# Kernel tuning notes

Hardware: AMD Instinct MI355X
Metric: run time of the kernel (lower is better)

## Reference

```python
import jax, jax.numpy as jnp
import numpy as np

N_EMBD = 1024
N_HEADS = 16
HEAD_DIM = N_EMBD // N_HEADS


def setup_inputs() -> dict:
    key = jax.random.key(0)
    ks = jax.random.split(key, 5)
    s = 0.02
    return {
        "x": jax.random.normal(ks[0], (4, 2048, N_EMBD), dtype=jnp.float32),
        "w_attn": jax.random.normal(ks[1], (N_EMBD, 3 * N_EMBD), dtype=jnp.float32) * s,
        "b_attn": jnp.zeros((3 * N_EMBD,), dtype=jnp.float32),
        "w_proj": jax.random.normal(ks[2], (N_EMBD, N_EMBD), dtype=jnp.float32) * s,
        "b_proj": jnp.zeros((N_EMBD,), dtype=jnp.float32),
    }


def reference(x, w_attn, b_attn, w_proj, b_proj):
    B, T, C = x.shape
    H, D = N_HEADS, HEAD_DIM
    qkv = x @ w_attn + b_attn                      # [B,T,3C]
    q, k, v = jnp.split(qkv, 3, axis=-1)
    q = q.reshape(B, T, H, D).transpose(0, 2, 1, 3)  # [B,H,T,D]
    k = k.reshape(B, T, H, D).transpose(0, 2, 1, 3)
    v = v.reshape(B, T, H, D).transpose(0, 2, 1, 3)
    # Faithful to source bug: divide by d**(-0.5) == multiply by sqrt(d)
    scale = jnp.asarray(D, x.dtype) ** 0.5
    scores = jnp.einsum("bhqd,bhkd->bhqk", q, k) * scale  # [B,H,T,T]
    causal = jnp.tril(jnp.ones((T, T), dtype=bool))
    scores = jnp.where(causal[None, None], scores, -jnp.inf)
    attn = jax.nn.softmax(scores, axis=-1)
    y = jnp.einsum("bhqk,bhkd->bhqd", attn, v)     # [B,H,T,D]
    y = y.transpose(0, 2, 1, 3).reshape(B, T, C)
    return y @ w_proj + b_proj
```

## Files before the change

### kernel.cpp

```cpp
#include <hip/hip_runtime.h>
#include <cmath>

#define BB 4
#define TT 2048
#define CC 1024
#define HH 16
#define DD 64
#define MM (BB*TT)

typedef _Float16 f16x8 __attribute__((ext_vector_type(8)));
typedef _Float16 f16x4 __attribute__((ext_vector_type(4)));
typedef _Float16 f16x2 __attribute__((ext_vector_type(2)));
typedef float f32x4 __attribute__((ext_vector_type(4)));
typedef unsigned short ushort_t;

#define MFMA16(a,b,c) __builtin_amdgcn_mfma_f32_16x16x16f16(a,b,c,0,0,0)

__device__ __forceinline__ unsigned short f2h(float f) {
    _Float16 h = (_Float16)f;
    return __builtin_bit_cast(unsigned short, h);
}

__device__ __forceinline__ f16x2 cvt_pk(float a, float b) {
    return __builtin_bit_cast(f16x2, __builtin_amdgcn_cvt_pkrtz(a, b));
}

__device__ __forceinline__ void gld16(const void* gsrc, void* ldst) {
    void* g = const_cast<void*>(gsrc);
    __builtin_amdgcn_global_load_lds(
        (__attribute__((address_space(1))) void*)g,
        (__attribute__((address_space(3))) void*)ldst,
        16, 0, 0);
}

__global__ __launch_bounds__(256)
void cvt4_kernel(const float* __restrict__ in, ushort_t* __restrict__ out, long n4) {
    long i = (long)blockIdx.x * blockDim.x + threadIdx.x;
    if (i >= n4) return;
    float4 v = ((const float4*)in)[i];
    ushort4 o;
    o.x = f2h(v.x); o.y = f2h(v.y); o.z = f2h(v.z); o.w = f2h(v.w);
    ((ushort4*)out)[i] = o;
}

__global__ __launch_bounds__(256)
void trcvt_kernel(const float* __restrict__ in, ushort_t* __restrict__ out,
                  int K, int N) {
    __shared__ float T[32][33];
    const int tx = threadIdx.x & 31;
    const int ty = threadIdx.x >> 5;
    const int n0 = blockIdx.x * 32;
    const int k0 = blockIdx.y * 32;
    #pragma unroll
    for (int i = 0; i < 4; ++i)
        T[ty + i * 8][tx] = in[(size_t)(k0 + ty + i * 8) * N + n0 + tx];
    __syncthreads();
    #pragma unroll
    for (int i = 0; i < 4; ++i)
        out[(size_t)(n0 + ty + i * 8) * K + k0 + tx] = f2h(T[tx][ty + i * 8]);
}

template<int N, bool QKV>
__global__ __launch_bounds__(256)
void hgemm_kernel(const ushort_t* __restrict__ A, const ushort_t* __restrict__ Bt,
                  const float* __restrict__ bias, float* __restrict__ out,
                  ushort_t* __restrict__ qh, ushort_t* __restrict__ kh,
                  ushort_t* __restrict__ vh)
{
    const int K = 1024;
    __shared__ ushort_t As[2][128 * 32];
    __shared__ ushort_t Bs[2][128 * 32];

    const int tid  = threadIdx.x;
    const int lane = tid & 63;
    const int wave = tid >> 6;
    const int wm   = (wave & 1) * 64;
    const int wn   = (wave >> 1) * 64;
    const int m0   = blockIdx.y * 128;
    const int n0   = blockIdx.x * 128;
    const int lrow = lane & 15;
    const int quad = lane >> 4;

    unsigned offA[4], offB[4];
    ushort_t* ldsA[4];
    ushort_t* ldsB[4];
    #pragma unroll
    for (int p = 0; p < 4; ++p) {
        const int d   = p * 256 + tid;
        const int blk = d >> 9;
        const int row = (d >> 2) & 127;
        const int c16 = d & 3;
        offA[p] = (unsigned)(m0 + row) * K + blk * 32 + c16 * 8;
        offB[p] = (unsigned)(n0 + row) * K + blk * 32 + c16 * 8;
        ldsA[p] = &As[0][0] + (p * 256 + wave * 64) * 8;
        ldsB[p] = &Bs[0][0] + (p * 256 + wave * 64) * 8;
    }

    f32x4 acc[4][4];
    const f32x4 z = {0.f, 0.f, 0.f, 0.f};
    #pragma unroll
    for (int mt = 0; mt < 4; ++mt)
        #pragma unroll
        for (int nt = 0; nt < 4; ++nt)
            acc[mt][nt] = z;

    for (int kk = 0; kk < K; kk += 64) {
        #pragma unroll
        for (int p = 0; p < 4; ++p) {
            gld16(&A[offA[p] + kk],  ldsA[p]);
            gld16(&Bt[offB[p] + kk], ldsB[p]);
        }
        __syncthreads();

        #pragma unroll
        for (int ks = 0; ks < 2; ++ks) {
            f16x8 af[4], bf[4];
            #pragma unroll
            for (int mt = 0; mt < 4; ++mt)
                af[mt] = *(const f16x8*)&As[ks][(wm + mt * 16 + lrow) * 32 + quad * 8];
            #pragma unroll
            for (int nt = 0; nt < 4; ++nt)
                bf[nt] = *(const f16x8*)&Bs[ks][(wn + nt * 16 + lrow) * 32 + quad * 8];
            #pragma unroll
            for (int mt = 0; mt < 4; ++mt)
                #pragma unroll
                for (int nt = 0; nt < 4; ++nt)
                    acc[mt][nt] = __builtin_amdgcn_mfma_f32_16x16x32_f16(
                        af[mt], bf[nt], acc[mt][nt], 0, 0, 0);
        }
        __syncthreads();
    }

    #pragma unroll
    for (int mt = 0; mt < 4; ++mt) {
        const int rbase = m0 + wm + mt * 16 + quad * 4;
        #pragma unroll
        for (int nt = 0; nt < 4; ++nt) {
            const int col = n0 + wn + nt * 16 + lrow;
            const float bv = bias[col];
            if (QKV) {
                const int which = col >> 10;
                const int c = col & 1023;
                const int h = c >> 6, d = c & 63;
                const int b = rbase >> 11, t0 = rbase & 2047;
                if (which == 2) {
                    ushort4 pk;
                    pk.x = f2h(acc[mt][nt][0] + bv);
                    pk.y = f2h(acc[mt][nt][1] + bv);
                    pk.z = f2h(acc[mt][nt][2] + bv);
                    pk.w = f2h(acc[mt][nt][3] + bv);
                    *(ushort4*)&vh[(((size_t)b * HH + h) * DD + d) * TT + t0] = pk;
                } else {
                    ushort_t* dst = which ? kh : qh;
                    const float sc = which ? 1.0f : 8.0f * 1.44269504088896f;
                    #pragma unroll
                    for (int r = 0; r < 4; ++r)
                        dst[(((size_t)b * HH + h) * TT + t0 + r) * DD + d] =
                            f2h((acc[mt][nt][r] + bv) * sc);
                }
            } else {
                #pragma unroll
                for (int r = 0; r < 4; ++r)
                    out[(size_t)(rbase + r) * N + col] = acc[mt][nt][r] + bv;
            }
        }
    }
}

__global__ __launch_bounds__(256, 4)
void attn_mfma_kernel(const ushort_t* __restrict__ qh, const ushort_t* __restrict__ kh,
                      const ushort_t* __restrict__ vh, ushort_t* __restrict__ yh)
{
    __shared__ ushort_t Ks[2][64 * 72];
    __shared__ ushort_t Vs[2][64 * 72];

    const int pr   = blockIdx.x;
    const int bh   = blockIdx.y;
    const int qtA  = 31 - pr;
    const int qtB  = pr;
    const int tid  = threadIdx.x;
    const int lane = tid & 63;
    const int w    = tid >> 6;
    const int lrow = lane & 15;
    const int quad = lane >> 4;

    const ushort_t* qbase = qh + (size_t)bh * TT * DD;
    const ushort_t* kbase = kh + (size_t)bh * TT * DD;
    const ushort_t* vbase = vh + (size_t)bh * DD * TT;
    const int b = bh >> 4, h = bh & 15;

    const int ur = tid >> 3;
    const int uc = (tid & 7) * 8;

    int q0w = qtA * 64 + w * 16;
    f16x8 aq0 = *(const f16x8*)&qbase[(size_t)(q0w + lrow) * DD + quad * 8];
    f16x8 aq1 = *(const f16x8*)&qbase[(size_t)(q0w + lrow) * DD + 32 + quad * 8];

    const f32x4 z = {0.f, 0.f, 0.f, 0.f};
    f32x4 o[4] = {z, z, z, z};
    float mi = -1e30f, li = 0.f;

    uint4 kr0 = *(const uint4*)&kbase[(size_t)ur * DD + uc];
    uint4 kr1 = *(const uint4*)&kbase[(size_t)(ur + 32) * DD + uc];
    uint4 vr0 = *(const uint4*)&vbase[(size_t)ur * TT + uc];
    uint4 vr1 = *(const uint4*)&vbase[(size_t)(ur + 32) * TT + uc];

    *(uint4*)&Ks[0][(ur)      * 72 + uc] = kr0;
    *(uint4*)&Ks[0][(ur + 32) * 72 + uc] = kr1;
    *(uint4*)&Vs[0][(ur)      * 72 + uc] = vr0;
    *(uint4*)&Vs[0][(ur + 32) * 72 + uc] = vr1;
    {
        const int nkt = (1 <= qtA) ? 1 : 0;
        const int nb  = nkt * 64;
        kr0 = *(const uint4*)&kbase[(size_t)(nb + ur) * DD + uc];
        kr1 = *(const uint4*)&kbase[(size_t)(nb + ur + 32) * DD + uc];
        vr0 = *(const uint4*)&vbase[(size_t)ur * TT + nb + uc];
        vr1 = *(const uint4*)&vbase[(size_t)(ur + 32) * TT + nb + uc];
    }
    __syncthreads();

    for (int i = 0; i <= 32; ++i) {
        const int cur = i & 1;
        if (i == qtA + 1) {
            #pragma unroll
            for (int r = 0; r < 4; ++r) {
                const float inv = 1.0f / __shfl(li, quad * 4 + r, 64);
                const int t = q0w + quad * 4 + r;
                #pragma unroll
                for (int dt = 0; dt < 4; ++dt)
                    yh[((size_t)b * TT + t) * CC + h * 64 + dt * 16 + lrow] =
                        f2h(o[dt][r] * inv);
            }
            q0w = qtB * 64 + w * 16;
            aq0 = *(const f16x8*)&qbase[(size_t)(q0w + lrow) * DD + quad * 8];
            aq1 = *(const f16x8*)&qbase[(size_t)(q0w + lrow) * DD + 32 + quad * 8];
            #pragma unroll
            for (int dt = 0; dt < 4; ++dt) o[dt] = z;
            mi = -1e30f; li = 0.f;
        }
        const int kt = (i <= qtA) ? i : i - qtA - 1;

        f32x4 sv[4];
        __builtin_amdgcn_s_setprio(1);
        #pragma unroll
        for (int c = 0; c < 4; ++c) {
            f16x8 ka = *(const f16x8*)&Ks[cur][(c * 16 + lrow) * 72 + quad * 8];
            f16x8 kb = *(const f16x8*)&Ks[cur][(c * 16 + lrow) * 72 + 32 + quad * 8];
            sv[c] = __builtin_amdgcn_mfma_f32_16x16x32_f16(ka, aq0, z, 0, 0, 0);
            sv[c] = __builtin_amdgcn_mfma_f32_16x16x32_f16(kb, aq1, sv[c], 0, 0, 0);
        }
        __builtin_amdgcn_s_setprio(0);

        const int kt2 = kt * 64;
        const int qg  = q0w + lrow;
        const bool diag = (i == qtA) || (i == 32);
        if (diag) {
            #pragma unroll
            for (int c = 0; c < 4; ++c)
                #pragma unroll
                for (int r = 0; r < 4; ++r)
                    if (kt2 + c * 16 + quad * 4 + r > qg) sv[c][r] = -3e38f;
        }
        float mc[4];
        #pragma unroll
        for (int c = 0; c < 4; ++c)
            mc[c] = fmaxf(fmaxf(sv[c][0], sv[c][1]), fmaxf(sv[c][2], sv[c][3]));
        float m = fmaxf(fmaxf(mc[0], mc[1]), fmaxf(mc[2], mc[3]));
        m = fmaxf(m, __shfl_xor(m, 16, 64));
        m = fmaxf(m, __shfl_xor(m, 32, 64));

        if (__any(m > mi + 8.0f)) {
            const float mnew  = fmaxf(mi, m);
            const float alpha = exp2f(mi - mnew);
            mi = mnew;
            li *= alpha;
            #pragma unroll
            for (int r = 0; r < 4; ++r) {
                const float ar = __shfl(alpha, quad * 4 + r, 64);
                #pragma unroll
                for (int dt = 0; dt < 4; ++dt) o[dt][r] *= ar;
            }
        }

        f16x4 ap[4];
        float rc[4];
        #pragma unroll
        for (int c = 0; c < 4; ++c) {
            const float p0 = exp2f(sv[c][0] - mi);
            const float p1 = exp2f(sv[c][1] - mi);
            const float p2 = exp2f(sv[c][2] - mi);
            const float p3 = exp2f(sv[c][3] - mi);
            rc[c] = (p0 + p1) + (p2 + p3);
            const f16x2 lo = cvt_pk(p0, p1);
            const f16x2 hi = cvt_pk(p2, p3);
            ap[c][0] = lo[0]; ap[c][1] = lo[1]; ap[c][2] = hi[0]; ap[c][3] = hi[1];
        }
        float rs = (rc[0] + rc[1]) + (rc[2] + rc[3]);
        rs += __shfl_xor(rs, 16, 64);
        rs += __shfl_xor(rs, 32, 64);
        li += rs;

        __builtin_amdgcn_s_setprio(1);
        #pragma unroll
        for (int dt = 0; dt < 4; ++dt)
            #pragma unroll
            for (int c = 0; c < 4; ++c) {
                f16x4 vb = *(const f16x4*)&Vs[cur][(dt * 16 + lrow) * 72 + c * 16 + quad * 4];
                o[dt] = MFMA16(ap[c], vb, o[dt]);
            }
        __builtin_amdgcn_s_setprio(0);

        if (i < 32) {
            const int nxt = cur ^ 1;
            *(uint4*)&Ks[nxt][(ur)      * 72 + uc] = kr0;
            *(uint4*)&Ks[nxt][(ur + 32) * 72 + uc] = kr1;
            *(uint4*)&Vs[nxt][(ur)      * 72 + uc] = vr0;
            *(uint4*)&Vs[nxt][(ur + 32) * 72 + uc] = vr1;
            if (i < 31) {
                const int ni  = i + 2;
                const int nkt = (ni <= qtA) ? ni : ni - qtA - 1;
                const int nb  = nkt * 64;
                kr0 = *(const uint4*)&kbase[(size_t)(nb + ur) * DD + uc];
                kr1 = *(const uint4*)&kbase[(size_t)(nb + ur + 32) * DD + uc];
                vr0 = *(const uint4*)&vbase[(size_t)ur * TT + nb + uc];
                vr1 = *(const uint4*)&vbase[(size_t)(ur + 32) * TT + nb + uc];
            }
        }
        __syncthreads();
    }

    #pragma unroll
    for (int r = 0; r < 4; ++r) {
        const float inv = 1.0f / __shfl(li, quad * 4 + r, 64);
        const int t = q0w + quad * 4 + r;
        #pragma unroll
        for (int dt = 0; dt < 4; ++dt)
            yh[((size_t)b * TT + t) * CC + h * 64 + dt * 16 + lrow] =
                f2h(o[dt][r] * inv);
    }
}

extern "C" void kernel_launch(void* const* d_in, const int* in_sizes, int n_in,
                              void* d_out, int out_size, void* d_ws, size_t ws_size,
                              hipStream_t stream) {
    const float* x      = (const float*)d_in[0];
    const float* w_attn = (const float*)d_in[1];
    const float* b_attn = (const float*)d_in[2];
    const float* w_proj = (const float*)d_in[3];
    const float* b_proj = (const float*)d_in[4];
    float* out = (float*)d_out;

    const size_t per = (size_t)BB * HH * TT * DD;
    ushort_t* qh  = (ushort_t*)d_ws;
    ushort_t* kh  = qh + per;
    ushort_t* vh  = kh + per;
    ushort_t* xh  = vh + per;
    ushort_t* yh  = xh;
    ushort_t* wat = xh + (size_t)MM * CC;
    ushort_t* wpt = wat + (size_t)3 * CC * CC;

    cvt4_kernel<<<(MM * CC / 4 + 255) / 256, 256, 0, stream>>>(x, xh, MM * CC / 4);
    trcvt_kernel<<<dim3(3 * CC / 32, CC / 32), 256, 0, stream>>>(w_attn, wat, CC, 3 * CC);
    trcvt_kernel<<<dim3(CC / 32, CC / 32), 256, 0, stream>>>(w_proj, wpt, CC, CC);

    hgemm_kernel<3 * CC, true><<<dim3(3 * CC / 128, MM / 128), 256, 0, stream>>>(
        xh, wat, b_attn, nullptr, qh, kh, vh);

    attn_mfma_kernel<<<dim3(16, BB * HH), 256, 0, stream>>>(qh, kh, vh, yh);

    hgemm_kernel<CC, false><<<dim3(CC / 128, MM / 128), 256, 0, stream>>>(
        yh, wpt, b_proj, out, nullptr, nullptr, nullptr);
}
```

Baseline: 279.8 us.

## Use 128-row query tiles with 8 waves per attention block

```diff
diff --git a/kernel.cpp b/kernel.cpp
--- a/kernel.cpp
+++ b/kernel.cpp
@@ -167,7 +167,7 @@
     }
 }
 
-__global__ __launch_bounds__(256, 4)
+__global__ __launch_bounds__(512, 4)
 void attn_mfma_kernel(const ushort_t* __restrict__ qh, const ushort_t* __restrict__ kh,
                       const ushort_t* __restrict__ vh, ushort_t* __restrict__ yh)
 {
@@ -176,8 +176,9 @@
 
     const int pr   = blockIdx.x;
     const int bh   = blockIdx.y;
-    const int qtA  = 31 - pr;
+    const int qtA  = 15 - pr;
     const int qtB  = pr;
+    const int itA  = 2 * qtA + 2;
     const int tid  = threadIdx.x;
     const int lane = tid & 63;
     const int w    = tid >> 6;
@@ -192,7 +193,7 @@
     const int ur = tid >> 3;
     const int uc = (tid & 7) * 8;
 
-    int q0w = qtA * 64 + w * 16;
+    int q0w = qtA * 128 + w * 16;
     f16x8 aq0 = *(const f16x8*)&qbase[(size_t)(q0w + lrow) * DD + quad * 8];
     f16x8 aq1 = *(const f16x8*)&qbase[(size_t)(q0w + lrow) * DD + 32 + quad * 8];
 
@@ -200,28 +201,18 @@
     f32x4 o[4] = {z, z, z, z};
     float mi = -1e30f, li = 0.f;
 
-    uint4 kr0 = *(const uint4*)&kbase[(size_t)ur * DD + uc];
-    uint4 kr1 = *(const uint4*)&kbase[(size_t)(ur + 32) * DD + uc];
-    uint4 vr0 = *(const uint4*)&vbase[(size_t)ur * TT + uc];
-    uint4 vr1 = *(const uint4*)&vbase[(size_t)(ur + 32) * TT + uc];
-
-    *(uint4*)&Ks[0][(ur)      * 72 + uc] = kr0;
-    *(uint4*)&Ks[0][(ur + 32) * 72 + uc] = kr1;
-    *(uint4*)&Vs[0][(ur)      * 72 + uc] = vr0;
-    *(uint4*)&Vs[0][(ur + 32) * 72 + uc] = vr1;
-    {
-        const int nkt = (1 <= qtA) ? 1 : 0;
-        const int nb  = nkt * 64;
-        kr0 = *(const uint4*)&kbase[(size_t)(nb + ur) * DD + uc];
-        kr1 = *(const uint4*)&kbase[(size_t)(nb + ur + 32) * DD + uc];
-        vr0 = *(const uint4*)&vbase[(size_t)ur * TT + nb + uc];
-        vr1 = *(const uint4*)&vbase[(size_t)(ur + 32) * TT + nb + uc];
-    }
+    uint4 kr = *(const uint4*)&kbase[(size_t)ur * DD + uc];
+    uint4 vr = *(const uint4*)&vbase[(size_t)ur * TT + uc];
+
+    *(uint4*)&Ks[0][ur * 72 + uc] = kr;
+    *(uint4*)&Vs[0][ur * 72 + uc] = vr;
+    kr = *(const uint4*)&kbase[(size_t)(64 + ur) * DD + uc];
+    vr = *(const uint4*)&vbase[(size_t)ur * TT + 64 + uc];
     __syncthreads();
 
-    for (int i = 0; i <= 32; ++i) {
+    for (int i = 0; i < 34; ++i) {
         const int cur = i & 1;
-        if (i == qtA + 1) {
+        if (i == itA) {
             #pragma unroll
             for (int r = 0; r < 4; ++r) {
                 const float inv = 1.0f / __shfl(li, quad * 4 + r, 64);
@@ -231,99 +222,95 @@
                     yh[((size_t)b * TT + t) * CC + h * 64 + dt * 16 + lrow] =
                         f2h(o[dt][r] * inv);
             }
-            q0w = qtB * 64 + w * 16;
+            q0w = qtB * 128 + w * 16;
             aq0 = *(const f16x8*)&qbase[(size_t)(q0w + lrow) * DD + quad * 8];
             aq1 = *(const f16x8*)&qbase[(size_t)(q0w + lrow) * DD + 32 + quad * 8];
             #pragma unroll
             for (int dt = 0; dt < 4; ++dt) o[dt] = z;
             mi = -1e30f; li = 0.f;
         }
-        const int kt = (i <= qtA) ? i : i - qtA - 1;
-
-        f32x4 sv[4];
-        __builtin_amdgcn_s_setprio(1);
-        #pragma unroll
-        for (int c = 0; c < 4; ++c) {
-            f16x8 ka = *(const f16x8*)&Ks[cur][(c * 16 + lrow) * 72 + quad * 8];
-            f16x8 kb = *(const f16x8*)&Ks[cur][(c * 16 + lrow) * 72 + 32 + quad * 8];
-            sv[c] = __builtin_amdgcn_mfma_f32_16x16x32_f16(ka, aq0, z, 0, 0, 0);
-            sv[c] = __builtin_amdgcn_mfma_f32_16x16x32_f16(kb, aq1, sv[c], 0, 0, 0);
-        }
-        __builtin_amdgcn_s_setprio(0);
-
+        const int kt = (i < itA) ? i : i - itA;
         const int kt2 = kt * 64;
-        const int qg  = q0w + lrow;
-        const bool diag = (i == qtA) || (i == 32);
-        if (diag) {
+        if (kt2 <= q0w + 15) {
+            f32x4 sv[4];
+            __builtin_amdgcn_s_setprio(1);
+            #pragma unroll
+            for (int c = 0; c < 4; ++c) {
+                f16x8 ka = *(const f16x8*)&Ks[cur][(c * 16 + lrow) * 72 + quad * 8];
+                f16x8 kb = *(const f16x8*)&Ks[cur][(c * 16 + lrow) * 72 + 32 + quad * 8];
+                sv[c] = __builtin_amdgcn_mfma_f32_16x16x32_f16(ka, aq0, z, 0, 0, 0);
+                sv[c] = __builtin_amdgcn_mfma_f32_16x16x32_f16(kb, aq1, sv[c], 0, 0, 0);
+            }
+            __builtin_amdgcn_s_setprio(0);
+
+            const int qg = q0w + lrow;
+            if (kt2 + 63 > q0w) {
+                #pragma unroll
+                for (int c = 0; c < 4; ++c)
+                    #pragma unroll
+                    for (int r = 0; r < 4; ++r)
+                        if (kt2 + c * 16 + quad * 4 + r > qg) sv[c][r] = -3e38f;
+            }
+            float mc[4];
             #pragma unroll
             for (int c = 0; c < 4; ++c)
-                #pragma unroll
-                for (int r = 0; r < 4; ++r)
-                    if (kt2 + c * 16 + quad * 4 + r > qg) sv[c][r] = -3e38f;
-        }
-        float mc[4];
-        #pragma unroll
-        for (int c = 0; c < 4; ++c)
-            mc[c] = fmaxf(fmaxf(sv[c][0], sv[c][1]), fmaxf(sv[c][2], sv[c][3]));
-        float m = fmaxf(fmaxf(mc[0], mc[1]), fmaxf(mc[2], mc[3]));
-        m = fmaxf(m, __shfl_xor(m, 16, 64));
-        m = fmaxf(m, __shfl_xor(m, 32, 64));
-
-        if (__any(m > mi + 8.0f)) {
-            const float mnew  = fmaxf(mi, m);
-            const float alpha = exp2f(mi - mnew);
-            mi = mnew;
-            li *= alpha;
-            #pragma unroll
-            for (int r = 0; r < 4; ++r) {
-                const float ar = __shfl(alpha, quad * 4 + r, 64);
-                #pragma unroll
-                for (int dt = 0; dt < 4; ++dt) o[dt][r] *= ar;
-            }
-        }
-
-        f16x4 ap[4];
-        float rc[4];
-        #pragma unroll
-        for (int c = 0; c < 4; ++c) {
-            const float p0 = exp2f(sv[c][0] - mi);
-            const float p1 = exp2f(sv[c][1] - mi);
-            const float p2 = exp2f(sv[c][2] - mi);
-            const float p3 = exp2f(sv[c][3] - mi);
-            rc[c] = (p0 + p1) + (p2 + p3);
-            const f16x2 lo = cvt_pk(p0, p1);
-            const f16x2 hi = cvt_pk(p2, p3);
-            ap[c][0] = lo[0]; ap[c][1] = lo[1]; ap[c][2] = hi[0]; ap[c][3] = hi[1];
-        }
-        float rs = (rc[0] + rc[1]) + (rc[2] + rc[3]);
-        rs += __shfl_xor(rs, 16, 64);
-        rs += __shfl_xor(rs, 32, 64);
-        li += rs;
-
-        __builtin_amdgcn_s_setprio(1);
-        #pragma unroll
-        for (int dt = 0; dt < 4; ++dt)
+                mc[c] = fmaxf(fmaxf(sv[c][0], sv[c][1]), fmaxf(sv[c][2], sv[c][3]));
+            float m = fmaxf(fmaxf(mc[0], mc[1]), fmaxf(mc[2], mc[3]));
+            m = fmaxf(m, __shfl_xor(m, 16, 64));
+            m = fmaxf(m, __shfl_xor(m, 32, 64));
+
+            if (__any(m > mi + 8.0f)) {
+                const float mnew  = fmaxf(mi, m);
+                const float alpha = exp2f(mi - mnew);
+                mi = mnew;
+                li *= alpha;
+                #pragma unroll
+                for (int r = 0; r < 4; ++r) {
+                    const float ar = __shfl(alpha, quad * 4 + r, 64);
+                    #pragma unroll
+                    for (int dt = 0; dt < 4; ++dt) o[dt][r] *= ar;
+                }
+            }
+
+            f16x4 ap[4];
+            float rc[4];
             #pragma unroll
             for (int c = 0; c < 4; ++c) {
-                f16x4 vb = *(const f16x4*)&Vs[cur][(dt * 16 + lrow) * 72 + c * 16 + quad * 4];
-                o[dt] = MFMA16(ap[c], vb, o[dt]);
-            }
-        __builtin_amdgcn_s_setprio(0);
-
-        if (i < 32) {
+                const float p0 = exp2f(sv[c][0] - mi);
+                const float p1 = exp2f(sv[c][1] - mi);
+                const float p2 = exp2f(sv[c][2] - mi);
+                const float p3 = exp2f(sv[c][3] - mi);
+                rc[c] = (p0 + p1) + (p2 + p3);
+                const f16x2 lo = cvt_pk(p0, p1);
+                const f16x2 hi = cvt_pk(p2, p3);
+                ap[c][0] = lo[0]; ap[c][1] = lo[1]; ap[c][2] = hi[0]; ap[c][3] = hi[1];
+            }
+            float rs = (rc[0] + rc[1]) + (rc[2] + rc[3]);
+            rs += __shfl_xor(rs, 16, 64);
+            rs += __shfl_xor(rs, 32, 64);
+            li += rs;
+
+            __builtin_amdgcn_s_setprio(1);
+            #pragma unroll
+            for (int dt = 0; dt < 4; ++dt)
+                #pragma unroll
+                for (int c = 0; c < 4; ++c) {
+                    f16x4 vb = *(const f16x4*)&Vs[cur][(dt * 16 + lrow) * 72 + c * 16 + quad * 4];
+                    o[dt] = MFMA16(ap[c], vb, o[dt]);
+                }
+            __builtin_amdgcn_s_setprio(0);
+        }
+
+        if (i < 33) {
             const int nxt = cur ^ 1;
-            *(uint4*)&Ks[nxt][(ur)      * 72 + uc] = kr0;
-            *(uint4*)&Ks[nxt][(ur + 32) * 72 + uc] = kr1;
-            *(uint4*)&Vs[nxt][(ur)      * 72 + uc] = vr0;
-            *(uint4*)&Vs[nxt][(ur + 32) * 72 + uc] = vr1;
-            if (i < 31) {
+            *(uint4*)&Ks[nxt][ur * 72 + uc] = kr;
+            *(uint4*)&Vs[nxt][ur * 72 + uc] = vr;
+            if (i < 32) {
                 const int ni  = i + 2;
-                const int nkt = (ni <= qtA) ? ni : ni - qtA - 1;
+                const int nkt = (ni < itA) ? ni : ni - itA;
                 const int nb  = nkt * 64;
-                kr0 = *(const uint4*)&kbase[(size_t)(nb + ur) * DD + uc];
-                kr1 = *(const uint4*)&kbase[(size_t)(nb + ur + 32) * DD + uc];
-                vr0 = *(const uint4*)&vbase[(size_t)ur * TT + nb + uc];
-                vr1 = *(const uint4*)&vbase[(size_t)(ur + 32) * TT + nb + uc];
+                kr = *(const uint4*)&kbase[(size_t)(nb + ur) * DD + uc];
+                vr = *(const uint4*)&vbase[(size_t)ur * TT + nb + uc];
             }
         }
         __syncthreads();
@@ -366,7 +353,7 @@
     hgemm_kernel<3 * CC, true><<<dim3(3 * CC / 128, MM / 128), 256, 0, stream>>>(
         xh, wat, b_attn, nullptr, qh, kh, vh);
 
-    attn_mfma_kernel<<<dim3(16, BB * HH), 256, 0, stream>>>(qh, kh, vh, yh);
+    attn_mfma_kernel<<<dim3(8, BB * HH), 512, 0, stream>>>(qh, kh, vh, yh);
 
     hgemm_kernel<CC, false><<<dim3(CC / 128, MM / 128), 256, 0, stream>>>(
         yh, wpt, b_proj, out, nullptr, nullptr, nullptr);
```

New measurement: 280.5 us. About the same (+0.3%).
